# Kernel tuning notes

Hardware: AMD Instinct MI355X
Metric: run time of the kernel (lower is better)

Reference implementation:

```python
import jax, jax.numpy as jnp
import numpy as np
import math

NUM_HEADS = 20
HEAD_SIZE = 20  # newssize = 400
NEG_INF = -1e9


def setup_inputs() -> dict:
    key = jax.random.key(0)
    ks = jax.random.split(key, 10)
    B, S, L, V, D, M = 512, 100, 30, 50000, 400, 128
    user_click = jax.random.randint(ks[0], (B, S, L), 0, V)
    seq_len = jax.random.randint(ks[1], (B,), 1, S + 1)  # at least 1 valid click
    sc = 1.0 / math.sqrt(D)
    return {
        "user_click": user_click,
        "seq_len": seq_len,
        "emb_table": jax.random.normal(ks[2], (V, D), jnp.float32) * 0.02,
        "wq": jax.random.normal(ks[3], (D, D), jnp.float32) * sc,
        "wk": jax.random.normal(ks[4], (D, D), jnp.float32) * sc,
        "wv": jax.random.normal(ks[5], (D, D), jnp.float32) * sc,
        "fc1_w": jax.random.normal(ks[6], (D, M), jnp.float32) * sc,
        "fc1_b": jnp.zeros((M,), jnp.float32),
        "fc2_w": jax.random.normal(ks[7], (M, 1), jnp.float32) * (1.0 / math.sqrt(M)),
        "fc2_b": jnp.zeros((1,), jnp.float32),
    }


def reference(user_click, seq_len, emb_table, wq, wk, wv, fc1_w, fc1_b, fc2_w, fc2_b):
    B, S, L = user_click.shape
    D = emb_table.shape[1]
    H, Dh = NUM_HEADS, HEAD_SIZE

    # news encoder: mean-pooled token embeddings -> [B, S, D]
    click = jnp.take(emb_table, user_click.reshape(-1, L), axis=0).mean(axis=1)
    click = click.reshape(B, S, D)

    # mask: valid positions get +1.0 (as in the torch code), invalid -1e9
    valid = jnp.arange(S)[None, :] < seq_len[:, None]  # [B, S]
    mask = jnp.where(valid, 1.0, NEG_INF).astype(click.dtype)

    # multi-head self-attention over history
    q = (click @ wq).reshape(B, S, H, Dh).transpose(0, 2, 1, 3)
    k = (click @ wk).reshape(B, S, H, Dh).transpose(0, 2, 1, 3)
    v = (click @ wv).reshape(B, S, H, Dh).transpose(0, 2, 1, 3)
    logits = jnp.einsum("bhqd,bhkd->bhqk", q, k) / math.sqrt(Dh)
    logits = logits + mask[:, None, None, :]
    attn = jax.nn.softmax(logits, axis=-1)
    ctx = jnp.einsum("bhqk,bhkd->bhqd", attn, v)
    ctx = ctx.transpose(0, 2, 1, 3).reshape(B, S, D)  # [B, S, D]

    # additive attention pooling over history positions
    e = jnp.tanh(ctx @ fc1_w + fc1_b)            # [B, S, M]
    alpha = e @ fc2_w + fc2_b + mask[:, :, None]  # [B, S, 1]
    w = jax.nn.softmax(alpha, axis=1)
    return jnp.sum(w * ctx, axis=1)               # [B, D]
```

## Files before the change

kernel.cpp:

```cpp
#include <hip/hip_runtime.h>
#include <hip/hip_bf16.h>

using u16 = unsigned short;
using u32 = unsigned int;

#define BB 512
#define SS 100
#define LL 30
#define DD 400
#define MM 128
#define HH 20
#define DHH 20
#define SLAB 1024000ull

typedef short v8s __attribute__((ext_vector_type(8)));
typedef float v4f __attribute__((ext_vector_type(4)));

__device__ __forceinline__ float lo2f(u32 u) { return __uint_as_float(u << 16); }
__device__ __forceinline__ float hi2f(u32 u) { return __uint_as_float(u & 0xffff0000u); }
__device__ __forceinline__ float bf2f(u16 h) { return __uint_as_float(((u32)h) << 16); }
__device__ __forceinline__ u16 f2bf(float f) {
  u32 u = __float_as_uint(f);
  u += 0x7fffu + ((u >> 16) & 1u);
  return (u16)(u >> 16);
}
__device__ __forceinline__ u32 packf2(float a, float b) {
  return (u32)f2bf(a) | (((u32)f2bf(b)) << 16);
}

__global__ __launch_bounds__(256) void k_cvt(const float* __restrict__ src,
                                             u16* __restrict__ dst, int n4) {
  const int i = blockIdx.x * 256 + threadIdx.x;
  if (i < n4) {
    const float4 v = ((const float4*)src)[i];
    ((uint2*)dst)[i] = make_uint2(packf2(v.x, v.y), packf2(v.z, v.w));
  }
}

__global__ __launch_bounds__(256) void k_trans(const float* __restrict__ src,
                                               u16* __restrict__ dst, int K, int N) {
  __shared__ float ts[32][33];
  const int t = threadIdx.x;
  const int n0 = blockIdx.x * 32, k0 = blockIdx.y * 32;
  const int c = t & 31, r8 = t >> 5;
#pragma unroll
  for (int i = 0; i < 4; ++i) {
    const int k = k0 + r8 + i * 8, n = n0 + c;
    ts[r8 + i * 8][c] = (k < K && n < N) ? src[(size_t)k * N + n] : 0.f;
  }
  __syncthreads();
#pragma unroll
  for (int i = 0; i < 4; ++i) {
    const int n = n0 + r8 + i * 8, k = k0 + c;
    if (n < N && k < K) dst[(size_t)n * K + k] = f2bf(ts[c][r8 + i * 8]);
  }
}

__global__ __launch_bounds__(256) void k_embed(const int* __restrict__ uc,
                                               const u16* __restrict__ emb,
                                               u32* __restrict__ click) {
  const int wave = threadIdx.x >> 6, lane = threadIdx.x & 63;
  const int bs = blockIdx.x * 4 + wave;
  __shared__ int rows[4][LL];
  if (lane < LL) rows[wave][lane] = uc[(size_t)bs * LL + lane];
  __syncthreads();
  float ax[4] = {0.f, 0.f, 0.f, 0.f}, ay[4] = {0.f, 0.f, 0.f, 0.f};
  for (int l = 0; l < LL; ++l) {
    const u32* row = (const u32*)(emb + (size_t)rows[wave][l] * DD);
    const u32 a = row[lane], b = row[lane + 64], c = row[lane + 128];
    ax[0] += lo2f(a); ay[0] += hi2f(a);
    ax[1] += lo2f(b); ay[1] += hi2f(b);
    ax[2] += lo2f(c); ay[2] += hi2f(c);
    if (lane < 8) { const u32 d = row[lane + 192]; ax[3] += lo2f(d); ay[3] += hi2f(d); }
  }
  const float s = 1.0f / (float)LL;
  u32* orow = click + (size_t)bs * 200;
  orow[lane]       = packf2(ax[0] * s, ay[0] * s);
  orow[lane + 64]  = packf2(ax[1] * s, ay[1] * s);
  orow[lane + 128] = packf2(ax[2] * s, ay[2] * s);
  if (lane < 8) orow[lane + 192] = packf2(ax[3] * s, ay[3] * s);
}

__global__ __launch_bounds__(256) void k_qkv_mfma(const u16* __restrict__ A,
    const u16* __restrict__ Wt, u16* __restrict__ qo, u16* __restrict__ ko_,
    u16* __restrict__ vo) {
  __shared__ u16 As[256][40];
  __shared__ u16 Bs[80][40];
  const int t = threadIdx.x;
  const int wave = t >> 6, lane = t & 63;
  const int q = lane >> 4, l16 = lane & 15;
  const int m0 = blockIdx.x * 256;
  const int mat = blockIdx.y / 5, ntile = blockIdx.y % 5;
  const int nb = ntile * 80;
  const u16* Bt = Wt + (size_t)(mat * 400 + nb) * 400;
  u16* O = (mat == 0) ? qo : ((mat == 1) ? ko_ : vo);
  const int mw = wave * 64;

  v4f acc[4][5];
#pragma unroll
  for (int i = 0; i < 4; ++i)
#pragma unroll
    for (int j = 0; j < 5; ++j) acc[i][j] = (v4f){0.f, 0.f, 0.f, 0.f};

  for (int kt = 0; kt < 13; ++kt) {
    const int k0 = kt * 32;
#pragma unroll
    for (int i = 0; i < 4; ++i) {
      const int id = i * 256 + t;
      const int r = id >> 2, ko = (id & 3) * 8;
      uint4 val = make_uint4(0u, 0u, 0u, 0u);
      if (k0 + ko < 400) val = *(const uint4*)&A[(size_t)(m0 + r) * 400 + k0 + ko];
      *(uint4*)&As[r][ko] = val;
    }
#pragma unroll
    for (int i = 0; i < 2; ++i) {
      const int id = i * 256 + t;
      if (id < 320) {
        const int n = id >> 2, ko = (id & 3) * 8;
        uint4 val = make_uint4(0u, 0u, 0u, 0u);
        if (k0 + ko < 400) val = *(const uint4*)&Bt[(size_t)n * 400 + k0 + ko];
        *(uint4*)&Bs[n][ko] = val;
      }
    }
    __syncthreads();
    v8s a[4], b[5];
#pragma unroll
    for (int ms = 0; ms < 4; ++ms) a[ms] = *(const v8s*)&As[mw + ms * 16 + l16][q * 8];
#pragma unroll
    for (int ns = 0; ns < 5; ++ns) b[ns] = *(const v8s*)&Bs[ns * 16 + l16][q * 8];
#pragma unroll
    for (int ms = 0; ms < 4; ++ms)
#pragma unroll
      for (int ns = 0; ns < 5; ++ns)
        acc[ms][ns] = __builtin_amdgcn_mfma_f32_16x16x32_bf16(a[ms], b[ns], acc[ms][ns], 0, 0, 0);
    __syncthreads();
  }
#pragma unroll
  for (int ms = 0; ms < 4; ++ms)
#pragma unroll
    for (int ns = 0; ns < 5; ++ns) {
      const v4f c = acc[ms][ns];
      const int col = nb + ns * 16 + l16;
      const int head = col / 20, dh = col % 20;
      u16* Oh = O + (size_t)head * SLAB + dh;
#pragma unroll
      for (int reg = 0; reg < 4; ++reg) {
        const int m = m0 + mw + ms * 16 + q * 4 + reg;
        Oh[(size_t)m * 20] = f2bf(c[reg]);
      }
    }
}

__global__ __launch_bounds__(256) void k_attn_mfma(const u16* __restrict__ qg,
    const u16* __restrict__ kg, const u16* __restrict__ vg,
    const int* __restrict__ seq, u16* __restrict__ ctxg) {
  __shared__ u16 Qs[112][40];
  __shared__ u16 Ks[112][40];
  __shared__ u16 Vs[112][40];
  __shared__ u16 Vt[32][136];
  __shared__ u16 Ss[112][136];
  const int b = blockIdx.x / HH, h = blockIdx.x % HH;
  const int t = threadIdx.x;
  const int wave = t >> 6, lane = t & 63;
  const int quad = lane >> 4, l16 = lane & 15;
  const int len = seq[b];
  const u16* qb = qg + (size_t)h * SLAB + (size_t)b * SS * DHH;
  const u16* kb = kg + (size_t)h * SLAB + (size_t)b * SS * DHH;
  const u16* vb = vg + (size_t)h * SLAB + (size_t)b * SS * DHH;
  for (int id = t; id < 896; id += 256) {
    const int r = id >> 3, ch = id & 7;
    uint2 vq = make_uint2(0u, 0u), vk = vq, vv = vq;
    if (r < 100 && ch < 5) {
      vq = *(const uint2*)(qb + r * DHH + ch * 4);
      vk = *(const uint2*)(kb + r * DHH + ch * 4);
      vv = *(const uint2*)(vb + r * DHH + ch * 4);
    }
    *(uint2*)&Qs[r][ch * 4] = vq;
    *(uint2*)&Ks[r][ch * 4] = vk;
    *(uint2*)&Vs[r][ch * 4] = vv;
  }
  for (int id = t; id < 816; id += 256) ((u32*)&Vt[20][0])[id] = 0u;
  for (int id = t; id < 360; id += 256) {
    const int r = id / 18, c = id % 18;
    *(u32*)&Vt[r][100 + c * 2] = 0u;
  }
  for (int id = t; id < 896; id += 256) {
    const int r = id >> 3, c = id & 7;
    *(u32*)&Ss[r][112 + c * 2] = 0u;
  }
  __syncthreads();
  for (int id = t; id < 2000; id += 256) {
    const int d = id / 100, key = id % 100;
    Vt[d][key] = Vs[key][d];
  }
  const float sc = 0.2236067977499790f;
  for (int mi = 0; mi < 2; ++mi) {
    const int mt = wave + mi * 4;
    if (mt >= 7) break;
    const v8s a = *(const v8s*)&Qs[mt * 16 + l16][quad * 8];
    v4f acc[7];
#pragma unroll
    for (int nt = 0; nt < 7; ++nt) {
      const v8s bk = *(const v8s*)&Ks[nt * 16 + l16][quad * 8];
      acc[nt] = __builtin_amdgcn_mfma_f32_16x16x32_bf16(a, bk, (v4f){0.f,0.f,0.f,0.f}, 0, 0, 0);
    }
#pragma unroll
    for (int reg = 0; reg < 4; ++reg) {
      float v[7];
      float mx = -3.0e38f;
#pragma unroll
      for (int nt = 0; nt < 7; ++nt) {
        const int col = nt * 16 + l16;
        v[nt] = acc[nt][reg] * sc + ((col < len) ? 1.0f : -1e9f);
        mx = fmaxf(mx, v[nt]);
      }
#pragma unroll
      for (int o = 1; o < 16; o <<= 1) mx = fmaxf(mx, __shfl_xor(mx, o));
      float sum = 0.f;
#pragma unroll
      for (int nt = 0; nt < 7; ++nt) { v[nt] = __expf(v[nt] - mx); sum += v[nt]; }
#pragma unroll
      for (int o = 1; o < 16; o <<= 1) sum += __shfl_xor(sum, o);
      const float inv = 1.0f / sum;
      const int row = mt * 16 + quad * 4 + reg;
#pragma unroll
      for (int nt = 0; nt < 7; ++nt) Ss[row][nt * 16 + l16] = f2bf(v[nt] * inv);
    }
  }
  __syncthreads();
  u16* cb = ctxg + (size_t)b * SS * DD + h * DHH;
  for (int mi = 0; mi < 2; ++mi) {
    const int mt = wave + mi * 4;
    if (mt >= 7) break;
    v4f o0 = (v4f){0.f,0.f,0.f,0.f}, o1 = o0;
#pragma unroll
    for (int kc = 0; kc < 4; ++kc) {
      const v8s a  = *(const v8s*)&Ss[mt * 16 + l16][kc * 32 + quad * 8];
      const v8s b0 = *(const v8s*)&Vt[l16][kc * 32 + quad * 8];
      const v8s b1 = *(const v8s*)&Vt[16 + l16][kc * 32 + quad * 8];
      o0 = __builtin_amdgcn_mfma_f32_16x16x32_bf16(a, b0, o0, 0, 0, 0);
      o1 = __builtin_amdgcn_mfma_f32_16x16x32_bf16(a, b1, o1, 0, 0, 0);
    }
#pragma unroll
    for (int reg = 0; reg < 4; ++reg) {
      const int q = mt * 16 + quad * 4 + reg;
      if (q < 100) {
        cb[(size_t)q * DD + l16] = f2bf(o0[reg]);
        if (l16 < 4) cb[(size_t)q * DD + 16 + l16] = f2bf(o1[reg]);
      }
    }
  }
}

__global__ __launch_bounds__(256) void k_fc1_mfma(const u16* __restrict__ A,
    const u16* __restrict__ Bt, const float* __restrict__ f1b,
    float* __restrict__ e) {
  __shared__ u16 As[128][40];
  __shared__ u16 Bs[64][40];
  const int t = threadIdx.x;
  const int wave = t >> 6, lane = t & 63;
  const int q = lane >> 4, l16 = lane & 15;
  const int m0 = blockIdx.x * 128;
  const int nb = blockIdx.y * 64;
  const int mw = wave * 32;
  v4f acc[2][4];
#pragma unroll
  for (int i = 0; i < 2; ++i)
#pragma unroll
    for (int j = 0; j < 4; ++j) acc[i][j] = (v4f){0.f, 0.f, 0.f, 0.f};

  for (int kt = 0; kt < 13; ++kt) {
    const int k0 = kt * 32;
#pragma unroll
    for (int i = 0; i < 2; ++i) {
      const int id = i * 256 + t;
      const int r = id >> 2, ko = (id & 3) * 8;
      uint4 val = make_uint4(0u, 0u, 0u, 0u);
      if (k0 + ko < 400) val = *(const uint4*)&A[(size_t)(m0 + r) * 400 + k0 + ko];
      *(uint4*)&As[r][ko] = val;
    }
    {
      const int r = t >> 2, ko = (t & 3) * 8;
      uint4 val = make_uint4(0u, 0u, 0u, 0u);
      if (k0 + ko < 400) val = *(const uint4*)&Bt[(size_t)(nb + r) * 400 + k0 + ko];
      *(uint4*)&Bs[r][ko] = val;
    }
    __syncthreads();
    v8s a[2], b[4];
#pragma unroll
    for (int ms = 0; ms < 2; ++ms) a[ms] = *(const v8s*)&As[mw + ms * 16 + l16][q * 8];
#pragma unroll
    for (int ns = 0; ns < 4; ++ns) b[ns] = *(const v8s*)&Bs[ns * 16 + l16][q * 8];
#pragma unroll
    for (int ms = 0; ms < 2; ++ms)
#pragma unroll
      for (int ns = 0; ns < 4; ++ns)
        acc[ms][ns] = __builtin_amdgcn_mfma_f32_16x16x32_bf16(a[ms], b[ns], acc[ms][ns], 0, 0, 0);
    __syncthreads();
  }
#pragma unroll
  for (int ms = 0; ms < 2; ++ms)
#pragma unroll
    for (int ns = 0; ns < 4; ++ns) {
      const v4f c = acc[ms][ns];
      const int col = nb + ns * 16 + l16;
      const float bias = f1b[col];
#pragma unroll
      for (int reg = 0; reg < 4; ++reg) {
        const int m = m0 + mw + ms * 16 + q * 4 + reg;
        e[(size_t)m * MM + col] = tanhf(c[reg] + bias);
      }
    }
}

__global__ __launch_bounds__(256) void k_pool(const float* __restrict__ e,
    const float* __restrict__ f2w, const float* __restrict__ f2b,
    const int* __restrict__ seq, const u16* __restrict__ ctxg,
    float* __restrict__ out) {
  const int b = blockIdx.x;
  const int t = threadIdx.x, w = t >> 6, lane = t & 63;
  __shared__ float wts[SS];
  __shared__ float fw[MM];
  if (t < MM) fw[t] = f2w[t];
  __syncthreads();
  const int len = seq[b];
  const float bias = f2b[0];
  for (int s = w; s < SS; s += 4) {
    const float* er = e + (size_t)(b * SS + s) * MM;
    float p = er[lane] * fw[lane] + er[lane + 64] * fw[lane + 64];
#pragma unroll
    for (int o = 32; o > 0; o >>= 1) p += __shfl_down(p, o);
    if (lane == 0) wts[s] = p + bias + ((s < len) ? 1.0f : -1e9f);
  }
  __syncthreads();
  if (w == 0) {
    const float v0 = wts[lane];
    const float v1 = (lane + 64 < SS) ? wts[lane + 64] : -3.0e38f;
    float mx = fmaxf(v0, v1);
#pragma unroll
    for (int o = 32; o > 0; o >>= 1) mx = fmaxf(mx, __shfl_xor(mx, o));
    const float e0 = __expf(v0 - mx);
    const float e1 = (lane + 64 < SS) ? __expf(v1 - mx) : 0.f;
    float sm = e0 + e1;
#pragma unroll
    for (int o = 32; o > 0; o >>= 1) sm += __shfl_xor(sm, o);
    const float inv = 1.0f / sm;
    wts[lane] = e0 * inv;
    if (lane + 64 < SS) wts[lane + 64] = e1 * inv;
  }
  __syncthreads();
  for (int d = t; d < DD; d += 256) {
    float acc = 0.f;
    const u16* cb = ctxg + (size_t)b * SS * DD + d;
    for (int s = 0; s < SS; ++s) acc += wts[s] * bf2f(cb[(size_t)s * DD]);
    out[(size_t)b * DD + d] = acc;
  }
}

extern "C" void kernel_launch(void* const* d_in, const int* in_sizes, int n_in,
                              void* d_out, int out_size, void* d_ws, size_t ws_size,
                              hipStream_t stream) {
  const int*   uc  = (const int*)d_in[0];
  const int*   seq = (const int*)d_in[1];
  const float* emb = (const float*)d_in[2];
  const float* wq  = (const float*)d_in[3];
  const float* wk  = (const float*)d_in[4];
  const float* wv  = (const float*)d_in[5];
  const float* f1w = (const float*)d_in[6];
  const float* f1b = (const float*)d_in[7];
  const float* f2w = (const float*)d_in[8];
  const float* f2b = (const float*)d_in[9];
  float* out = (float*)d_out;

  u16* emb16   = (u16*)d_ws;
  u16* wt      = emb16 + 20000000ull;
  u16* wtf     = wt + 480000ull;
  u16* click16 = wtf + 51200ull;
  u16* q16     = click16 + 20480000ull;
  u16* k16     = q16 + 20480000ull;
  u16* v16     = k16 + 20480000ull;
  float* e     = (float*)q16;

  k_cvt<<<(5000000 + 255) / 256, 256, 0, stream>>>(emb, emb16, 5000000);
  k_trans<<<dim3(13, 13), 256, 0, stream>>>(wq, wt, 400, 400);
  k_trans<<<dim3(13, 13), 256, 0, stream>>>(wk, wt + 160000, 400, 400);
  k_trans<<<dim3(13, 13), 256, 0, stream>>>(wv, wt + 320000, 400, 400);
  k_trans<<<dim3(4, 13), 256, 0, stream>>>(f1w, wtf, 400, 128);
  k_embed<<<12800, 256, 0, stream>>>(uc, emb16, (u32*)click16);
  k_qkv_mfma<<<dim3(200, 15), 256, 0, stream>>>(click16, wt, q16, k16, v16);
  k_attn_mfma<<<BB * HH, 256, 0, stream>>>(q16, k16, v16, seq, click16);
  k_fc1_mfma<<<dim3(400, 2), 256, 0, stream>>>(click16, wtf, f1b, e);
  k_pool<<<BB, 256, 0, stream>>>(e, f2w, f2b, seq, click16, out);
}
```

Before: 660.4 us.

## Fuse fc2 projection into fc1 epilogue, prefetch embedding table, merge transposes

The fc1 MFMA kernel now applies tanh, multiplies by fc2 weights and reduces across columns, atomically accumulating per-row alpha scores instead of writing the full e activation tensor; the pool kernel reads alpha directly. A new warm kernel zeroes alpha and streams the bf16 embedding table to warm caches before the gather. The four weight transposes are merged into one launch. Atomics add nondeterministic summation order and the warm pass costs extra bandwidth.

```diff
diff --git a/kernel.cpp b/kernel.cpp
--- a/kernel.cpp
+++ b/kernel.cpp
@@ -37,9 +37,29 @@
   }
 }
 
-__global__ __launch_bounds__(256) void k_trans(const float* __restrict__ src,
-                                               u16* __restrict__ dst, int K, int N) {
+__global__ __launch_bounds__(256) void k_warm(const uint4* __restrict__ emb16,
+                                              int n16, float* __restrict__ alpha,
+                                              int nA, float* __restrict__ sink) {
+  const int gid = blockIdx.x * 256 + threadIdx.x;
+  const int stride = gridDim.x * 256;
+  for (int i = gid; i < nA; i += stride) alpha[i] = 0.f;
+  u32 s = 0;
+  for (int i = gid; i < n16; i += stride) {
+    const uint4 v = emb16[i];
+    s += v.x ^ v.y ^ v.z ^ v.w;
+  }
+  if (s == 0x12345678u) sink[0] = 1.f;
+}
+
+__global__ __launch_bounds__(256) void k_trans_all(const float* __restrict__ wq,
+    const float* __restrict__ wk, const float* __restrict__ wv,
+    const float* __restrict__ f1w, u16* __restrict__ wt, u16* __restrict__ wtf) {
   __shared__ float ts[32][33];
+  const int z = blockIdx.z;
+  const float* src = (z == 0) ? wq : (z == 1) ? wk : (z == 2) ? wv : f1w;
+  u16* dst = (z < 3) ? (wt + (size_t)z * 160000) : wtf;
+  const int N = (z < 3) ? 400 : 128;
+  const int K = 400;
   const int t = threadIdx.x;
   const int n0 = blockIdx.x * 32, k0 = blockIdx.y * 32;
   const int c = t & 31, r8 = t >> 5;
@@ -252,14 +272,14 @@
   }
 }
 
-__global__ __launch_bounds__(256) void k_fc1_mfma(const u16* __restrict__ A,
+__global__ __launch_bounds__(256) void k_fc1_alpha(const u16* __restrict__ A,
     const u16* __restrict__ Bt, const float* __restrict__ f1b,
-    float* __restrict__ e) {
+    const float* __restrict__ f2w, float* __restrict__ alpha) {
   __shared__ u16 As[128][40];
   __shared__ u16 Bs[64][40];
   const int t = threadIdx.x;
   const int wave = t >> 6, lane = t & 63;
-  const int q = lane >> 4, l16 = lane & 15;
+  const int quad = lane >> 4, l16 = lane & 15;
   const int m0 = blockIdx.x * 128;
   const int nb = blockIdx.y * 64;
   const int mw = wave * 32;
@@ -288,9 +308,9 @@
     __syncthreads();
     v8s a[2], b[4];
 #pragma unroll
-    for (int ms = 0; ms < 2; ++ms) a[ms] = *(const v8s*)&As[mw + ms * 16 + l16][q * 8];
-#pragma unroll
-    for (int ns = 0; ns < 4; ++ns) b[ns] = *(const v8s*)&Bs[ns * 16 + l16][q * 8];
+    for (int ms = 0; ms < 2; ++ms) a[ms] = *(const v8s*)&As[mw + ms * 16 + l16][quad * 8];
+#pragma unroll
+    for (int ns = 0; ns < 4; ++ns) b[ns] = *(const v8s*)&Bs[ns * 16 + l16][quad * 8];
 #pragma unroll
     for (int ms = 0; ms < 2; ++ms)
 #pragma unroll
@@ -298,40 +318,36 @@
         acc[ms][ns] = __builtin_amdgcn_mfma_f32_16x16x32_bf16(a[ms], b[ns], acc[ms][ns], 0, 0, 0);
     __syncthreads();
   }
+  float fwv[4], fbv[4];
+#pragma unroll
+  for (int ns = 0; ns < 4; ++ns) {
+    fwv[ns] = f2w[nb + ns * 16 + l16];
+    fbv[ns] = f1b[nb + ns * 16 + l16];
+  }
 #pragma unroll
   for (int ms = 0; ms < 2; ++ms)
 #pragma unroll
-    for (int ns = 0; ns < 4; ++ns) {
-      const v4f c = acc[ms][ns];
-      const int col = nb + ns * 16 + l16;
-      const float bias = f1b[col];
-#pragma unroll
-      for (int reg = 0; reg < 4; ++reg) {
-        const int m = m0 + mw + ms * 16 + q * 4 + reg;
-        e[(size_t)m * MM + col] = tanhf(c[reg] + bias);
-      }
-    }
-}
-
-__global__ __launch_bounds__(256) void k_pool(const float* __restrict__ e,
-    const float* __restrict__ f2w, const float* __restrict__ f2b,
-    const int* __restrict__ seq, const u16* __restrict__ ctxg,
-    float* __restrict__ out) {
+    for (int reg = 0; reg < 4; ++reg) {
+      float p = 0.f;
+#pragma unroll
+      for (int ns = 0; ns < 4; ++ns)
+        p += tanhf(acc[ms][ns][reg] + fbv[ns]) * fwv[ns];
+#pragma unroll
+      for (int o = 1; o < 16; o <<= 1) p += __shfl_xor(p, o);
+      if (l16 == 0)
+        atomicAdd(&alpha[m0 + mw + ms * 16 + quad * 4 + reg], p);
+    }
+}
+
+__global__ __launch_bounds__(256) void k_pool(const float* __restrict__ alpha,
+    const float* __restrict__ f2b, const int* __restrict__ seq,
+    const u16* __restrict__ ctxg, float* __restrict__ out) {
   const int b = blockIdx.x;
   const int t = threadIdx.x, w = t >> 6, lane = t & 63;
   __shared__ float wts[SS];
-  __shared__ float fw[MM];
-  if (t < MM) fw[t] = f2w[t];
-  __syncthreads();
   const int len = seq[b];
   const float bias = f2b[0];
-  for (int s = w; s < SS; s += 4) {
-    const float* er = e + (size_t)(b * SS + s) * MM;
-    float p = er[lane] * fw[lane] + er[lane + 64] * fw[lane + 64];
-#pragma unroll
-    for (int o = 32; o > 0; o >>= 1) p += __shfl_down(p, o);
-    if (lane == 0) wts[s] = p + bias + ((s < len) ? 1.0f : -1e9f);
-  }
+  if (t < SS) wts[t] = alpha[b * SS + t] + bias + ((t < len) ? 1.0f : -1e9f);
   __syncthreads();
   if (w == 0) {
     const float v0 = wts[lane];
@@ -379,16 +395,15 @@
   u16* q16     = click16 + 20480000ull;
   u16* k16     = q16 + 20480000ull;
   u16* v16     = k16 + 20480000ull;
-  float* e     = (float*)q16;
+  float* alpha = (float*)(v16 + 20480000ull);
+  float* sink  = alpha + 51200ull;
 
   k_cvt<<<(5000000 + 255) / 256, 256, 0, stream>>>(emb, emb16, 5000000);
-  k_trans<<<dim3(13, 13), 256, 0, stream>>>(wq, wt, 400, 400);
-  k_trans<<<dim3(13, 13), 256, 0, stream>>>(wk, wt + 160000, 400, 400);
-  k_trans<<<dim3(13, 13), 256, 0, stream>>>(wv, wt + 320000, 400, 400);
-  k_trans<<<dim3(4, 13), 256, 0, stream>>>(f1w, wtf, 400, 128);
+  k_warm<<<2560, 256, 0, stream>>>((const uint4*)emb16, 2500000, alpha, 51200, sink);
+  k_trans_all<<<dim3(13, 13, 4), 256, 0, stream>>>(wq, wk, wv, f1w, wt, wtf);
   k_embed<<<12800, 256, 0, stream>>>(uc, emb16, (u32*)click16);
   k_qkv_mfma<<<dim3(200, 15), 256, 0, stream>>>(click16, wt, q16, k16, v16);
   k_attn_mfma<<<BB * HH, 256, 0, stream>>>(q16, k16, v16, seq, click16);
-  k_fc1_mfma<<<dim3(400, 2), 256, 0, stream>>>(click16, wtf, f1b, e);
-  k_pool<<<BB, 256, 0, stream>>>(e, f2w, f2b, seq, click16, out);
-}
+  k_fc1_alpha<<<dim3(400, 2), 256, 0, stream>>>(click16, wtf, f1b, f2w, alpha);
+  k_pool<<<BB, 256, 0, stream>>>(alpha, f2b, seq, click16, out);
+}
```

After: 642.4 us. 1.03x faster.
